# Kernel tuning notes

Measured on AMD Instinct MI355X. Metric: run time of the kernel, lower is better.

## Reference

```python
import jax, jax.numpy as jnp
import numpy as np

N_NODES = 100000
N_EDGES = 1600000
N_GRAPHS = 256
NEG_SLOPE_GAT = 0.2   # GATConv default
NEG_SLOPE_ACT = 0.01  # F.leaky_relu default


def _leaky(x, s):
    return jnp.where(x >= 0, x, s * x)


def _gat_layer(x, src, dst, W, a_src, a_dst, b, n):
    # h = W x ; per-node attention logits
    h = x @ W                      # [N, D]
    al_s = h @ a_src               # [N]
    al_d = h @ a_dst               # [N]
    e = _leaky(al_s[src] + al_d[dst], NEG_SLOPE_GAT)  # [E]
    # segment softmax over incoming edges of each dst node
    m = jax.ops.segment_max(e, dst, num_segments=n)
    m = jnp.where(jnp.isfinite(m), m, 0.0)
    ex = jnp.exp(e - m[dst])
    s = jax.ops.segment_sum(ex, dst, num_segments=n)
    alpha = ex / (s[dst] + 1e-16)
    out = jax.ops.segment_sum(h[src] * alpha[:, None], dst, num_segments=n)
    return out + b


def setup_inputs() -> dict:
    key = jax.random.key(0)
    ks = jax.random.split(key, 12)
    x = jax.random.normal(ks[0], (N_NODES, 72), dtype=jnp.float32)
    edge_index = jax.random.randint(ks[1], (2, N_EDGES), 0, N_NODES, dtype=jnp.int64)
    batch = jnp.sort(jax.random.randint(ks[2], (N_NODES,), 0, N_GRAPHS, dtype=jnp.int64))
    def glorot(k, shape):
        fan = shape[0] + shape[-1]
        return jax.random.normal(k, shape, dtype=jnp.float32) * jnp.sqrt(2.0 / fan)
    return {
        "x": x, "edge_index": edge_index, "batch": batch,
        "W1": glorot(ks[3], (72, 64)),
        "a_src1": glorot(ks[4], (64,)), "a_dst1": glorot(ks[5], (64,)),
        "b1": jnp.zeros((64,), jnp.float32),
        "W2": glorot(ks[6], (64, 64)),
        "a_src2": glorot(ks[7], (64,)), "a_dst2": glorot(ks[8], (64,)),
        "b2": jnp.zeros((64,), jnp.float32),
        "fcW": glorot(ks[9], (64, 2)),
        "fcb": jnp.zeros((2,), jnp.float32),
    }


def reference(x, edge_index, batch, W1, a_src1, a_dst1, b1, W2, a_src2, a_dst2, b2, fcW, fcb):
    n = x.shape[0]
    # PyG GATConv adds self-loops by default
    loops = jnp.arange(n, dtype=edge_index.dtype)
    src = jnp.concatenate([edge_index[0], loops])
    dst = jnp.concatenate([edge_index[1], loops])
    h = _gat_layer(x, src, dst, W1, a_src1, a_dst1, b1, n)
    h = _leaky(h, NEG_SLOPE_ACT)
    h = _gat_layer(h, src, dst, W2, a_src2, a_dst2, b2, n)
    # global mean pool over graphs
    sums = jax.ops.segment_sum(h, batch, num_segments=N_GRAPHS)
    cnt = jax.ops.segment_sum(jnp.ones((n,), h.dtype), batch, num_segments=N_GRAPHS)
    pooled = sums / jnp.maximum(cnt, 1.0)[:, None]
    # dropout is identity at inference
    return pooled @ fcW + fcb
```

## Files before the change

### kernel.cpp

```cpp
#include <hip/hip_runtime.h>
#include <hip/hip_bf16.h>
#include <math.h>


#define NPB 256
#define EPB 4096
#define PSTRIDE 4608

__device__ __forceinline__ void atomAddF(float* a, float v) {
    unsafeAtomicAdd(a, v);
}

__device__ __forceinline__ unsigned int f2bf(float v) {
    unsigned int b = __float_as_uint(v);
    b += 0x7FFFu + ((b >> 16) & 1u);
    return b >> 16;
}

__global__ __launch_bounds__(256) void init_all(float* __restrict__ pooled,
                                                float* __restrict__ cnt,
                                                int* __restrict__ bcur,
                                                int NB, int G) {
    int i = blockIdx.x * 256 + threadIdx.x;
    if (i < G * 64) pooled[i] = 0.0f;
    if (i < G) cnt[i] = 0.0f;
    if (i < NB) bcur[i] = 0;
}

__global__ __launch_bounds__(256) void partition(const int* __restrict__ ei,
                                                 int E, int NB,
                                                 int* __restrict__ bcur,
                                                 uint2* __restrict__ pairs) {
    __shared__ int h[512];
    __shared__ int hb[512];
    int t = threadIdx.x;
    for (int i = t; i < 512; i += 256) h[i] = 0;
    __syncthreads();
    int i0 = blockIdx.x * EPB;
    int s[16], bk[16], r[16];
#pragma unroll
    for (int k = 0; k < 16; k++) {
        int i = i0 + k * 256 + t;
        bk[k] = -1;
        if (i < E) {
            s[k] = ei[i];
            int d = ei[E + i];
            bk[k] = d >> 8;
            r[k] = atomicAdd(&h[bk[k]], 1);
        }
    }
    __syncthreads();
    for (int b = t; b < NB; b += 256)
        hb[b] = h[b] ? atomicAdd(&bcur[b], h[b]) : 0;
    __syncthreads();
#pragma unroll
    for (int k = 0; k < 16; k++) {
        if (bk[k] < 0) continue;
        int i = i0 + k * 256 + t;
        int d = ei[E + i];
        int pos = hb[bk[k]] + r[k];
        if (pos < PSTRIDE)
            pairs[(size_t)bk[k] * PSTRIDE + pos] =
                make_uint2((unsigned)s[k], (unsigned)d);
    }
}

__global__ __launch_bounds__(256) void build_csr(const uint2* __restrict__ pairs,
                                                 const int* __restrict__ bcur,
                                                 int n, int NB,
                                                 int* __restrict__ rowptr,
                                                 int* __restrict__ srcs) {
    int b = blockIdx.x, t = threadIdx.x;
    __shared__ int c[512];
    __shared__ int s2[256];
    __shared__ int sbase, stot;
    int c0 = (2 * t < NB) ? min(bcur[2 * t], PSTRIDE) : 0;
    int c1 = (2 * t + 1 < NB) ? min(bcur[2 * t + 1], PSTRIDE) : 0;
    c[2 * t] = c0; c[2 * t + 1] = c1;
    s2[t] = c0 + c1;
    __syncthreads();
    for (int o = 1; o < 256; o <<= 1) {
        int u = (t >= o) ? s2[t - o] : 0;
        __syncthreads();
        s2[t] += u;
        __syncthreads();
    }
    if (t == 0) {
        int p = b >> 1;
        int ex = s2[p] - (c[2 * p] + c[2 * p + 1]);
        sbase = ex + ((b & 1) ? c[b & ~1] : 0);
        stot = s2[255];
    }
    __syncthreads();
    int d0 = b << 8;
    int nb = min(NPB, n - d0);
    int cnt_b = c[b];
    int csr0 = sbase + d0;
    const uint2* pb = pairs + (size_t)b * PSTRIDE;

    __shared__ int deg[NPB];
    __shared__ int cur[NPB];
    __shared__ int tmp[NPB];
    deg[t] = (t < nb) ? 1 : 0;
    __syncthreads();
    for (int j = t; j < cnt_b; j += 256)
        atomicAdd(&deg[pb[j].y - d0], 1);
    __syncthreads();
    int v = deg[t];
    tmp[t] = v;
    __syncthreads();
    for (int o = 1; o < NPB; o <<= 1) {
        int u = (t >= o) ? tmp[t - o] : 0;
        __syncthreads();
        tmp[t] += u;
        __syncthreads();
    }
    int excl = tmp[t] - v;
    if (t < nb) {
        rowptr[d0 + t] = csr0 + excl;
        srcs[csr0 + excl] = d0 + t;
        cur[t] = excl + 1;
    }
    __syncthreads();
    for (int j = t; j < cnt_b; j += 256) {
        uint2 p = pb[j];
        int off = atomicAdd(&cur[p.y - d0], 1);
        srcs[csr0 + off] = (int)p.x;
    }
    if (b == 0 && t == 0) rowptr[n] = n + stot;
}

template <int IN_DIM>
__global__ __launch_bounds__(256) void node_gemm(const float* __restrict__ x,
                                                 const float* __restrict__ W,
                                                 const float* __restrict__ a_src,
                                                 const float* __restrict__ a_dst,
                                                 const float* __restrict__ bias_in,
                                                 float slope_in,
                                                 unsigned short* __restrict__ h16,
                                                 float* __restrict__ al_s,
                                                 float* __restrict__ al_d,
                                                 int n) {
    __shared__ float Ws[IN_DIM * 64];
    __shared__ float xs[IN_DIM][64];
    int t = threadIdx.x;
    int nbase = blockIdx.x * 64;

    for (int idx = t; idx < IN_DIM * 16; idx += 256)
        ((float4*)Ws)[idx] = ((const float4*)W)[idx];
    for (int idx = t; idx < IN_DIM * 64; idx += 256) {
        int node = nbase + (idx & 63);
        int k = idx >> 6;
        float v = 0.0f;
        if (node < n) {
            v = x[(size_t)node * IN_DIM + k];
            if (bias_in) {
                v += bias_in[k];
                v = (v >= 0.0f) ? v : slope_in * v;
            }
        }
        xs[k][idx & 63] = v;
    }
    __syncthreads();

    int cg = t & 15;
    int ng = t >> 4;
    float acc[4][4] = {};
#pragma unroll 8
    for (int k = 0; k < IN_DIM; k++) {
        float4 xv = *(const float4*)&xs[k][ng * 4];
        float4 wv = *(const float4*)&Ws[k * 64 + cg * 4];
        float xa[4] = {xv.x, xv.y, xv.z, xv.w};
        float wa[4] = {wv.x, wv.y, wv.z, wv.w};
#pragma unroll
        for (int i = 0; i < 4; i++)
#pragma unroll
            for (int j = 0; j < 4; j++)
                acc[i][j] += xa[i] * wa[j];
    }

    float4 as4 = *(const float4*)(a_src + cg * 4);
    float4 ad4 = *(const float4*)(a_dst + cg * 4);
#pragma unroll
    for (int i = 0; i < 4; i++) {
        int node = nbase + ng * 4 + i;
        if (node < n) {
            uint2 p;
            p.x = f2bf(acc[i][0]) | (f2bf(acc[i][1]) << 16);
            p.y = f2bf(acc[i][2]) | (f2bf(acc[i][3]) << 16);
            *(uint2*)(h16 + (size_t)node * 64 + cg * 4) = p;
        }
        float vs = acc[i][0] * as4.x + acc[i][1] * as4.y +
                   acc[i][2] * as4.z + acc[i][3] * as4.w;
        float vd = acc[i][0] * ad4.x + acc[i][1] * ad4.y +
                   acc[i][2] * ad4.z + acc[i][3] * ad4.w;
#pragma unroll
        for (int o = 8; o; o >>= 1) {
            vs += __shfl_xor(vs, o);
            vd += __shfl_xor(vd, o);
        }
        if (cg == 0 && node < n) { al_s[node] = vs; al_d[node] = vd; }
    }
}

__device__ __forceinline__ void bf8_fma(float* acc, uint4 q, float w) {
    acc[0] += w * __uint_as_float(q.x << 16);
    acc[1] += w * __uint_as_float(q.x & 0xFFFF0000u);
    acc[2] += w * __uint_as_float(q.y << 16);
    acc[3] += w * __uint_as_float(q.y & 0xFFFF0000u);
    acc[4] += w * __uint_as_float(q.z << 16);
    acc[5] += w * __uint_as_float(q.z & 0xFFFF0000u);
    acc[6] += w * __uint_as_float(q.w << 16);
    acc[7] += w * __uint_as_float(q.w & 0xFFFF0000u);
}

__global__ __launch_bounds__(256) void gat_aggregate(const int* __restrict__ rowptr,
                                                     const int* __restrict__ srcs,
                                                     const float* __restrict__ als,
                                                     const float* __restrict__ ald,
                                                     const unsigned short* __restrict__ h16,
                                                     float* __restrict__ hout,
                                                     int n) {
    int t = threadIdx.x;
    int sub = t >> 3, lane = t & 7;
    int node = blockIdx.x * 32 + sub;
    if (node >= n) return;
    int beg = rowptr[node], end = rowptr[node + 1];
    float aldv = ald[node];
    const unsigned short* hb = h16 + lane * 8;

    float acc[8] = {};
    float sm = 0.0f;
    int j = beg;
    for (; j + 8 <= end; j += 8) {
        int s[8];
        uint4 q[8];
        float e[8];
#pragma unroll
        for (int k = 0; k < 8; k++) s[k] = srcs[j + k];
#pragma unroll
        for (int k = 0; k < 8; k++) q[k] = *(const uint4*)(hb + (size_t)s[k] * 64);
#pragma unroll
        for (int k = 0; k < 8; k++) e[k] = als[s[k]] + aldv;
#pragma unroll
        for (int k = 0; k < 8; k++) {
            float ek = (e[k] >= 0.0f) ? e[k] : 0.2f * e[k];
            float w = __expf(ek);
            sm += w;
            bf8_fma(acc, q[k], w);
        }
    }
    for (; j < end; j++) {
        int s = srcs[j];
        float e = als[s] + aldv;
        e = (e >= 0.0f) ? e : 0.2f * e;
        float w = __expf(e);
        uint4 q = *(const uint4*)(hb + (size_t)s * 64);
        sm += w;
        bf8_fma(acc, q, w);
    }

    float inv = 1.0f / (sm + 1e-16f);
    float4 o0 = make_float4(acc[0] * inv, acc[1] * inv, acc[2] * inv, acc[3] * inv);
    float4 o1 = make_float4(acc[4] * inv, acc[5] * inv, acc[6] * inv, acc[7] * inv);
    float* op = hout + (size_t)node * 64 + lane * 8;
    *(float4*)op = o0;
    *(float4*)(op + 4) = o1;
}

__global__ __launch_bounds__(256) void pool_run(const float* __restrict__ hout,
                                                const float* __restrict__ b2,
                                                const int* __restrict__ batch,
                                                float* __restrict__ pooled,
                                                float* __restrict__ cnt,
                                                int n) {
    int t = threadIdx.x;
    int wv = blockIdx.x * 4 + (t >> 6);
    int lane = t & 63;
    int start = wv * 64;
    if (start >= n) return;
    int end = min(start + 64, n);
    float bb = b2[lane];
    int gcur = batch[start];
    float acc = 0.0f;
    int rl = 0;
    for (int node = start; node < end; node++) {
        int g = batch[node];
        if (g != gcur) {
            atomAddF(&pooled[gcur * 64 + lane], acc);
            if (lane == 0) atomAddF(&cnt[gcur], (float)rl);
            acc = 0.0f; rl = 0; gcur = g;
        }
        acc += hout[(size_t)node * 64 + lane] + bb;
        rl++;
    }
    atomAddF(&pooled[gcur * 64 + lane], acc);
    if (lane == 0) atomAddF(&cnt[gcur], (float)rl);
}

__global__ __launch_bounds__(64) void final_fc(const float* __restrict__ pooled,
                                               const float* __restrict__ cnt,
                                               const float* __restrict__ fcW,
                                               const float* __restrict__ fcb,
                                               float* __restrict__ out) {
    int g = blockIdx.x;
    int lane = threadIdx.x;
    float c = cnt[g];
    c = (c > 1.0f) ? c : 1.0f;
    float p = pooled[g * 64 + lane] / c;
    float s0 = p * fcW[lane * 2 + 0];
    float s1 = p * fcW[lane * 2 + 1];
#pragma unroll
    for (int o = 32; o; o >>= 1) {
        s0 += __shfl_xor(s0, o);
        s1 += __shfl_xor(s1, o);
    }
    if (lane == 0) {
        out[g * 2 + 0] = s0 + fcb[0];
        out[g * 2 + 1] = s1 + fcb[1];
    }
}

extern "C" void kernel_launch(void* const* d_in, const int* in_sizes, int n_in,
                              void* d_out, int out_size, void* d_ws, size_t ws_size,
                              hipStream_t stream) {
    const float* x    = (const float*)d_in[0];
    const int*   ei   = (const int*)d_in[1];
    const int*   batch= (const int*)d_in[2];
    const float* W1   = (const float*)d_in[3];
    const float* as1  = (const float*)d_in[4];
    const float* ad1  = (const float*)d_in[5];
    const float* b1   = (const float*)d_in[6];
    const float* W2   = (const float*)d_in[7];
    const float* as2  = (const float*)d_in[8];
    const float* ad2  = (const float*)d_in[9];
    const float* b2   = (const float*)d_in[10];
    const float* fcW  = (const float*)d_in[11];
    const float* fcb  = (const float*)d_in[12];
    float* out = (float*)d_out;

    const int N = in_sizes[2];
    const int E = in_sizes[1] / 2;
    const int G = out_size / 2;
    const int tot = E + N;
    const int NB = (N + NPB - 1) / NPB;

    float* ws     = (float*)d_ws;
    float* bufO   = ws;
    uint2* pairs  = (uint2*)(bufO + (size_t)N * 64);
    float* als    = (float*)(pairs + (size_t)NB * PSTRIDE);
    float* ald    = als + N;
    float* pooled = ald + N;
    float* cnt    = pooled + (size_t)G * 64;
    int*   rowptr = (int*)(cnt + G);
    int*   srcs   = rowptr + N + 1;
    int*   bcur   = srcs + tot;
    unsigned short* bufH16 = (unsigned short*)(bcur + NB);

    dim3 b256(256);
    int gInit = (max(G * 64, NB) + 255) / 256;
    int gPart = (E + EPB - 1) / EPB;
    int gGemm = (N + 63) / 64;
    int gAgg  = (N + 31) / 32;
    int gPool = ((N + 63) / 64 + 3) / 4;

    init_all<<<gInit, b256, 0, stream>>>(pooled, cnt, bcur, NB, G);
    partition<<<gPart, b256, 0, stream>>>(ei, E, NB, bcur, pairs);
    build_csr<<<NB, b256, 0, stream>>>(pairs, bcur, N, NB, rowptr, srcs);

    node_gemm<72><<<gGemm, b256, 0, stream>>>(x, W1, as1, ad1, nullptr, 0.0f,
                                              bufH16, als, ald, N);
    gat_aggregate<<<gAgg, b256, 0, stream>>>(rowptr, srcs, als, ald, bufH16, bufO, N);

    node_gemm<64><<<gGemm, b256, 0, stream>>>(bufO, W2, as2, ad2, b1, 0.01f,
                                              bufH16, als, ald, N);
    gat_aggregate<<<gAgg, b256, 0, stream>>>(rowptr, srcs, als, ald, bufH16, bufO, N);

    pool_run<<<gPool, b256, 0, stream>>>(bufO, b2, batch, pooled, cnt, N);
    final_fc<<<G, 64, 0, stream>>>(pooled, cnt, fcW, fcb, out);
}
```

Baseline: 338.1 us.

## Fuse pooling with FC, halve partition tile, split aggregation launches, unroll by four

Replaces the atomic-based pool_run and final_fc with one pool_fc kernel. Each block binary-searches the sorted batch array for its graph's node range and reduces it directly, so the pooled and count buffers and their zeroing go away. The partition kernel now handles 2048 edges per block instead of 4096. Each GAT aggregation is split into two launches over node halves, and its inner loop is unrolled by four instead of eight to cut register pressure. These trade an extra launch per layer and more partition blocks for fewer atomics and possibly higher occupancy.

Result: slower. 375.1 us (+10.9%).

```diff
diff --git a/kernel.cpp b/kernel.cpp
--- a/kernel.cpp
+++ b/kernel.cpp
@@ -4,12 +4,8 @@
 
 
 #define NPB 256
-#define EPB 4096
+#define EPB 2048
 #define PSTRIDE 4608
-
-__device__ __forceinline__ void atomAddF(float* a, float v) {
-    unsafeAtomicAdd(a, v);
-}
 
 __device__ __forceinline__ unsigned int f2bf(float v) {
     unsigned int b = __float_as_uint(v);
@@ -17,13 +13,8 @@
     return b >> 16;
 }
 
-__global__ __launch_bounds__(256) void init_all(float* __restrict__ pooled,
-                                                float* __restrict__ cnt,
-                                                int* __restrict__ bcur,
-                                                int NB, int G) {
+__global__ __launch_bounds__(256) void init_all(int* __restrict__ bcur, int NB) {
     int i = blockIdx.x * 256 + threadIdx.x;
-    if (i < G * 64) pooled[i] = 0.0f;
-    if (i < G) cnt[i] = 0.0f;
     if (i < NB) bcur[i] = 0;
 }
 
@@ -37,9 +28,9 @@
     for (int i = t; i < 512; i += 256) h[i] = 0;
     __syncthreads();
     int i0 = blockIdx.x * EPB;
-    int s[16], bk[16], r[16];
-#pragma unroll
-    for (int k = 0; k < 16; k++) {
+    int s[8], bk[8], r[8];
+#pragma unroll
+    for (int k = 0; k < 8; k++) {
         int i = i0 + k * 256 + t;
         bk[k] = -1;
         if (i < E) {
@@ -54,7 +45,7 @@
         hb[b] = h[b] ? atomicAdd(&bcur[b], h[b]) : 0;
     __syncthreads();
 #pragma unroll
-    for (int k = 0; k < 16; k++) {
+    for (int k = 0; k < 8; k++) {
         if (bk[k] < 0) continue;
         int i = i0 + k * 256 + t;
         int d = ei[E + i];
@@ -220,11 +211,11 @@
                                                      const float* __restrict__ ald,
                                                      const unsigned short* __restrict__ h16,
                                                      float* __restrict__ hout,
-                                                     int n) {
+                                                     int n0, int n1) {
     int t = threadIdx.x;
     int sub = t >> 3, lane = t & 7;
-    int node = blockIdx.x * 32 + sub;
-    if (node >= n) return;
+    int node = n0 + blockIdx.x * 32 + sub;
+    if (node >= n1) return;
     int beg = rowptr[node], end = rowptr[node + 1];
     float aldv = ald[node];
     const unsigned short* hb = h16 + lane * 8;
@@ -232,23 +223,25 @@
     float acc[8] = {};
     float sm = 0.0f;
     int j = beg;
-    for (; j + 8 <= end; j += 8) {
-        int s[8];
-        uint4 q[8];
-        float e[8];
-#pragma unroll
-        for (int k = 0; k < 8; k++) s[k] = srcs[j + k];
-#pragma unroll
-        for (int k = 0; k < 8; k++) q[k] = *(const uint4*)(hb + (size_t)s[k] * 64);
-#pragma unroll
-        for (int k = 0; k < 8; k++) e[k] = als[s[k]] + aldv;
-#pragma unroll
-        for (int k = 0; k < 8; k++) {
-            float ek = (e[k] >= 0.0f) ? e[k] : 0.2f * e[k];
-            float w = __expf(ek);
-            sm += w;
-            bf8_fma(acc, q[k], w);
-        }
+    for (; j + 4 <= end; j += 4) {
+        int s0 = srcs[j], s1 = srcs[j + 1], s2 = srcs[j + 2], s3 = srcs[j + 3];
+        float e0 = als[s0] + aldv, e1 = als[s1] + aldv;
+        float e2 = als[s2] + aldv, e3 = als[s3] + aldv;
+        uint4 q0 = *(const uint4*)(hb + (size_t)s0 * 64);
+        uint4 q1 = *(const uint4*)(hb + (size_t)s1 * 64);
+        uint4 q2 = *(const uint4*)(hb + (size_t)s2 * 64);
+        uint4 q3 = *(const uint4*)(hb + (size_t)s3 * 64);
+        e0 = (e0 >= 0.0f) ? e0 : 0.2f * e0;
+        e1 = (e1 >= 0.0f) ? e1 : 0.2f * e1;
+        e2 = (e2 >= 0.0f) ? e2 : 0.2f * e2;
+        e3 = (e3 >= 0.0f) ? e3 : 0.2f * e3;
+        float w0 = __expf(e0), w1 = __expf(e1);
+        float w2 = __expf(e2), w3 = __expf(e3);
+        sm += (w0 + w1) + (w2 + w3);
+        bf8_fma(acc, q0, w0);
+        bf8_fma(acc, q1, w1);
+        bf8_fma(acc, q2, w2);
+        bf8_fma(acc, q3, w3);
     }
     for (; j < end; j++) {
         int s = srcs[j];
@@ -268,56 +261,50 @@
     *(float4*)(op + 4) = o1;
 }
 
-__global__ __launch_bounds__(256) void pool_run(const float* __restrict__ hout,
-                                                const float* __restrict__ b2,
-                                                const int* __restrict__ batch,
-                                                float* __restrict__ pooled,
-                                                float* __restrict__ cnt,
-                                                int n) {
-    int t = threadIdx.x;
-    int wv = blockIdx.x * 4 + (t >> 6);
-    int lane = t & 63;
-    int start = wv * 64;
-    if (start >= n) return;
-    int end = min(start + 64, n);
-    float bb = b2[lane];
-    int gcur = batch[start];
-    float acc = 0.0f;
-    int rl = 0;
-    for (int node = start; node < end; node++) {
-        int g = batch[node];
-        if (g != gcur) {
-            atomAddF(&pooled[gcur * 64 + lane], acc);
-            if (lane == 0) atomAddF(&cnt[gcur], (float)rl);
-            acc = 0.0f; rl = 0; gcur = g;
-        }
-        acc += hout[(size_t)node * 64 + lane] + bb;
-        rl++;
-    }
-    atomAddF(&pooled[gcur * 64 + lane], acc);
-    if (lane == 0) atomAddF(&cnt[gcur], (float)rl);
-}
-
-__global__ __launch_bounds__(64) void final_fc(const float* __restrict__ pooled,
-                                               const float* __restrict__ cnt,
+__global__ __launch_bounds__(256) void pool_fc(const float* __restrict__ hout,
+                                               const float* __restrict__ b2,
+                                               const int* __restrict__ batch,
                                                const float* __restrict__ fcW,
                                                const float* __restrict__ fcb,
-                                               float* __restrict__ out) {
+                                               float* __restrict__ out, int n) {
     int g = blockIdx.x;
-    int lane = threadIdx.x;
-    float c = cnt[g];
-    c = (c > 1.0f) ? c : 1.0f;
-    float p = pooled[g * 64 + lane] / c;
-    float s0 = p * fcW[lane * 2 + 0];
-    float s1 = p * fcW[lane * 2 + 1];
-#pragma unroll
-    for (int o = 32; o; o >>= 1) {
-        s0 += __shfl_xor(s0, o);
-        s1 += __shfl_xor(s1, o);
-    }
-    if (lane == 0) {
-        out[g * 2 + 0] = s0 + fcb[0];
-        out[g * 2 + 1] = s1 + fcb[1];
+    int t = threadIdx.x;
+    __shared__ int sLo, sHi;
+    __shared__ float red[4][64];
+    if (t == 0) {
+        int lo = 0, hi = n;
+        while (lo < hi) { int m = (lo + hi) >> 1; if (batch[m] < g) lo = m + 1; else hi = m; }
+        sLo = lo;
+    } else if (t == 64) {
+        int lo = 0, hi = n;
+        while (lo < hi) { int m = (lo + hi) >> 1; if (batch[m] < g + 1) lo = m + 1; else hi = m; }
+        sHi = lo;
+    }
+    __syncthreads();
+    int lo = sLo, hi = sHi;
+    int wv = t >> 6, lane = t & 63;
+    float acc = 0.0f;
+    for (int node = lo + wv; node < hi; node += 4)
+        acc += hout[(size_t)node * 64 + lane];
+    red[wv][lane] = acc;
+    __syncthreads();
+    if (wv == 0) {
+        float c = (float)(hi - lo);
+        float s = red[0][lane] + red[1][lane] + red[2][lane] + red[3][lane];
+        s += c * b2[lane];
+        float cd = (c > 1.0f) ? c : 1.0f;
+        float p = s / cd;
+        float s0 = p * fcW[lane * 2 + 0];
+        float s1 = p * fcW[lane * 2 + 1];
+#pragma unroll
+        for (int o = 32; o; o >>= 1) {
+            s0 += __shfl_xor(s0, o);
+            s1 += __shfl_xor(s1, o);
+        }
+        if (lane == 0) {
+            out[g * 2 + 0] = s0 + fcb[0];
+            out[g * 2 + 1] = s1 + fcb[1];
+        }
     }
 }
 
@@ -350,32 +337,32 @@
     uint2* pairs  = (uint2*)(bufO + (size_t)N * 64);
     float* als    = (float*)(pairs + (size_t)NB * PSTRIDE);
     float* ald    = als + N;
-    float* pooled = ald + N;
-    float* cnt    = pooled + (size_t)G * 64;
-    int*   rowptr = (int*)(cnt + G);
+    int*   rowptr = (int*)(ald + N);
     int*   srcs   = rowptr + N + 1;
     int*   bcur   = srcs + tot;
     unsigned short* bufH16 = (unsigned short*)(bcur + NB);
 
     dim3 b256(256);
-    int gInit = (max(G * 64, NB) + 255) / 256;
+    int gInit = (NB + 255) / 256;
     int gPart = (E + EPB - 1) / EPB;
     int gGemm = (N + 63) / 64;
-    int gAgg  = (N + 31) / 32;
-    int gPool = ((N + 63) / 64 + 3) / 4;
-
-    init_all<<<gInit, b256, 0, stream>>>(pooled, cnt, bcur, NB, G);
+    int H = (((N + 1) / 2 + 31) / 32) * 32;
+    int gAgg1 = (H + 31) / 32;
+    int gAgg2 = (N - H + 31) / 32;
+
+    init_all<<<gInit, b256, 0, stream>>>(bcur, NB);
     partition<<<gPart, b256, 0, stream>>>(ei, E, NB, bcur, pairs);
     build_csr<<<NB, b256, 0, stream>>>(pairs, bcur, N, NB, rowptr, srcs);
 
     node_gemm<72><<<gGemm, b256, 0, stream>>>(x, W1, as1, ad1, nullptr, 0.0f,
                                               bufH16, als, ald, N);
-    gat_aggregate<<<gAgg, b256, 0, stream>>>(rowptr, srcs, als, ald, bufH16, bufO, N);
+    gat_aggregate<<<gAgg1, b256, 0, stream>>>(rowptr, srcs, als, ald, bufH16, bufO, 0, H);
+    gat_aggregate<<<gAgg2, b256, 0, stream>>>(rowptr, srcs, als, ald, bufH16, bufO, H, N);
 
     node_gemm<64><<<gGemm, b256, 0, stream>>>(bufO, W2, as2, ad2, b1, 0.01f,
                                               bufH16, als, ald, N);
-    gat_aggregate<<<gAgg, b256, 0, stream>>>(rowptr, srcs, als, ald, bufH16, bufO, N);
-
-    pool_run<<<gPool, b256, 0, stream>>>(bufO, b2, batch, pooled, cnt, N);
-    final_fc<<<G, 64, 0, stream>>>(pooled, cnt, fcW, fcb, out);
-}
+    gat_aggregate<<<gAgg1, b256, 0, stream>>>(rowptr, srcs, als, ald, bufH16, bufO, 0, H);
+    gat_aggregate<<<gAgg2, b256, 0, stream>>>(rowptr, srcs, als, ald, bufH16, bufO, H, N);
+
+    pool_fc<<<G, b256, 0, stream>>>(bufO, b2, batch, fcW, fcb, out, N);
+}
```
